# Optimization experiments

Measured on AMD Instinct MI355X. Metric: run time of the kernel, lower is better.

The kernel has to match this reference:

```python
import jax, jax.numpy as jnp
import numpy as np

D_MODEL = 1024

def setup_inputs() -> dict:
    key = jax.random.key(0)
    ks = jax.random.split(key, 7)
    B, T, D = 4, 4096, D_MODEL
    s = 1.0 / np.sqrt(D)
    return {
        "x": jax.random.normal(ks[0], (B, T, D), dtype=jnp.float32),
        "Wq": jax.random.normal(ks[1], (D, D), dtype=jnp.float32) * s,
        "bq": jax.random.normal(ks[2], (D,), dtype=jnp.float32) * 0.01,
        "Wk": jax.random.normal(ks[3], (D, D), dtype=jnp.float32) * s,
        "bk": jax.random.normal(ks[4], (D,), dtype=jnp.float32) * 0.01,
        "Wv": jax.random.normal(ks[5], (D, D), dtype=jnp.float32) * s,
        "bv": jax.random.normal(ks[6], (D,), dtype=jnp.float32) * 0.01,
    }

def reference(x, Wq, bq, Wk, bk, Wv, bv):
    # x: [B, T, D]; Linear weights stored [out, in] like torch -> x @ W.T + b
    D = x.shape[-1]
    T = x.shape[1]
    scale = jnp.sqrt(jnp.asarray(D, dtype=x.dtype))
    Q = jnp.einsum('btd,ed->bte', x, Wq) + bq
    K = jnp.einsum('btd,ed->bte', x, Wk) + bk
    V = jnp.einsum('btd,ed->bte', x, Wv) + bv
    scores = jnp.einsum('bqd,bkd->bqk', Q, K) / scale  # [B, T, T]
    causal = jnp.tril(jnp.ones((T, T), dtype=bool))    # True = keep (q >= k)
    neg_inf = jnp.asarray(-jnp.inf, dtype=scores.dtype)
    scores = jnp.where(causal, scores, neg_inf)
    probs = jax.nn.softmax(scores, axis=-1)
    return jnp.einsum('bqk,bkd->bqd', probs, V)
```

## Files before the change

### kernel.cpp

```cpp
#include <hip/hip_runtime.h>
#include <hip/hip_bf16.h>
#include <math.h>


typedef __bf16 bf16;
typedef __bf16 bf16x8 __attribute__((ext_vector_type(8)));
typedef float  f32x4  __attribute__((ext_vector_type(4)));

#define LOG2E 1.4426950408889634f

static constexpr size_t OFF_XB   = 0;
static constexpr size_t OFF_WQB  = 33554432;
static constexpr size_t OFF_WKB  = 35651584;
static constexpr size_t OFF_WVB  = 37748736;
static constexpr size_t OFF_Q    = 39845888;
static constexpr size_t OFF_K    = 73400320;
static constexpr size_t OFF_VT   = 106954752;
static constexpr size_t OFF_S    = 140509184;
static constexpr size_t OFF_PSUM = 209715200;
static constexpr size_t OFF_LINV = 211812352;

typedef __attribute__((address_space(1))) void gvoid_t;
typedef __attribute__((address_space(3))) void lvoid_t;

__device__ __forceinline__ void gload16(const void* g, void* l) {
  __builtin_amdgcn_global_load_lds((gvoid_t*)g, (lvoid_t*)l, 16, 0, 0);
}

#define PRIO1() __builtin_amdgcn_s_setprio(1)
#define PRIO0() __builtin_amdgcn_s_setprio(0)
#define BARF()  asm volatile("s_barrier" ::: "memory")
#define SB0()   __builtin_amdgcn_sched_barrier(0)
#define VM0()   asm volatile("s_waitcnt vmcnt(0)" ::: "memory")
#define VM4()   asm volatile("s_waitcnt vmcnt(4)" ::: "memory")

struct Ctx { int tid, lane, quad, col16, wr, wc, wcol; };
__device__ __forceinline__ Ctx mk_ctx() {
  Ctx c; c.tid = (int)threadIdx.x; c.lane = c.tid & 63;
  int w = c.tid >> 6;
  c.quad = c.lane >> 4; c.col16 = c.lane & 15;
  c.wr = (w >> 1) * 64; c.wc = (w & 1) * 64; c.wcol = w & 1;
  return c;
}

__device__ __forceinline__ void stage_tile(const bf16* g, long ld, bf16* s, int tid) {
  int lane = tid & 63, w = tid >> 6;
  const bf16* gp = g + (long)(lane >> 2) * ld + (long)(lane & 3) * 8;
  long step = 16 * ld;
  gload16(gp + (long)(2 * w) * step,     s + (2 * w) * 512);
  gload16(gp + (long)(2 * w + 1) * step, s + (2 * w + 1) * 512);
}

__device__ __forceinline__ void mfma_step(const bf16* sA, const bf16* sB,
                                          const Ctx& c, f32x4 acc[4][4]) {
  bf16x8 a[4], b[4];
#pragma unroll
  for (int i = 0; i < 4; ++i) {
    a[i] = *(const bf16x8*)(sA + ((c.wr + i * 16 + c.col16) * 32 + c.quad * 8));
    b[i] = *(const bf16x8*)(sB + ((c.wc + i * 16 + c.col16) * 32 + c.quad * 8));
  }
#pragma unroll
  for (int i = 0; i < 4; ++i)
#pragma unroll
    for (int j = 0; j < 4; ++j)
      acc[i][j] = __builtin_amdgcn_mfma_f32_16x16x32_bf16(a[i], b[j], acc[i][j], 0, 0, 0);
}

__device__ __forceinline__ void zero_acc(f32x4 acc[4][4]) {
  f32x4 z = {0.f, 0.f, 0.f, 0.f};
#pragma unroll
  for (int i = 0; i < 4; ++i)
#pragma unroll
    for (int j = 0; j < 4; ++j) acc[i][j] = z;
}

__device__ __forceinline__ int tridec(int i) {
  int qt = (int)((sqrtf(8.0f * (float)i + 1.0f) - 1.0f) * 0.5f);
  while ((qt + 1) * (qt + 2) / 2 <= i) ++qt;
  while (qt * (qt + 1) / 2 > i) --qt;
  return qt;
}

struct CC { int soff, ra0, ra1, rb0, rb1, lofs; };
__device__ __forceinline__ CC mk_cc(int tid) {
  CC c;
  int lane = tid & 63, w = tid >> 6;
  int quad = lane >> 4, col16 = lane & 15;
  int wrow = (w >> 2) << 7, wcol = (w & 3) << 6;
  int c7 = col16 & 7;
  c.soff = ((tid >> 3) << 10) + (((tid & 7) ^ ((tid >> 3) & 7)) << 3);
  c.ra0 = ((wrow + col16) << 6) + ((quad ^ c7) << 3);
  c.ra1 = ((wrow + col16) << 6) + (((4 | quad) ^ c7) << 3);
  c.rb0 = ((wcol + col16) << 6) + ((quad ^ c7) << 3);
  c.rb1 = ((wcol + col16) << 6) + (((4 | quad) ^ c7) << 3);
  c.lofs = w << 9;
  return c;
}

__device__ __forceinline__ void stg(const bf16* g, int kofs, bf16* l, const CC& c) {
  const bf16* g0 = g + kofs + c.soff;
  gload16(g0,         l + c.lofs);
  gload16(g0 + 65536, l + c.lofs + 4096);
}

__device__ __forceinline__ void read_a(const bf16* buf, const CC& c, int h, bf16x8 a[8]) {
#pragma unroll
  for (int f = 0; f < 4; ++f) {
    a[f * 2 + 0] = *(const bf16x8*)(buf + c.ra0 + h * 4096 + f * 1024);
    a[f * 2 + 1] = *(const bf16x8*)(buf + c.ra1 + h * 4096 + f * 1024);
  }
}

__device__ __forceinline__ void read_b(const bf16* buf, const CC& c, int cc, bf16x8 bb[4]) {
#pragma unroll
  for (int g = 0; g < 2; ++g) {
    bb[g * 2 + 0] = *(const bf16x8*)(buf + c.rb0 + cc * 2048 + g * 1024);
    bb[g * 2 + 1] = *(const bf16x8*)(buf + c.rb1 + cc * 2048 + g * 1024);
  }
}

__device__ __forceinline__ void read_ab(const bf16* bufA, const bf16* bufB,
                                        const CC& c, bf16x8 a[8], bf16x8 bb[4]) {
#pragma unroll
  for (int f = 0; f < 4; ++f) {
    a[f * 2 + 0] = *(const bf16x8*)(bufA + c.ra0 + f * 1024);
    a[f * 2 + 1] = *(const bf16x8*)(bufA + c.ra1 + f * 1024);
    if (f < 2) {
      bb[f * 2 + 0] = *(const bf16x8*)(bufB + c.rb0 + f * 1024);
      bb[f * 2 + 1] = *(const bf16x8*)(bufB + c.rb1 + f * 1024);
    }
  }
}

__device__ __forceinline__ void mfma16(const bf16x8 a[8], const bf16x8 bb[4],
                                       int h, int cc, f32x4 acc[8][4]) {
#pragma unroll
  for (int f = 0; f < 4; ++f)
#pragma unroll
    for (int g = 0; g < 2; ++g)
#pragma unroll
      for (int kk = 0; kk < 2; ++kk)
        acc[h * 4 + f][cc * 2 + g] = __builtin_amdgcn_mfma_f32_16x16x32_bf16(
            a[f * 2 + kk], bb[g * 2 + kk], acc[h * 4 + f][cc * 2 + g], 0, 0, 0);
}

__device__ __forceinline__ void zero8x4(f32x4 acc[8][4]) {
  f32x4 z = {0.f, 0.f, 0.f, 0.f};
#pragma unroll
  for (int i = 0; i < 8; ++i)
#pragma unroll
    for (int j = 0; j < 4; ++j) acc[i][j] = z;
}

template <int NT>
__device__ __forceinline__ void gemm256_core(const bf16* __restrict__ Ag,
                                             const bf16* __restrict__ Bg,
                                             bf16* sA0, bf16* sA1,
                                             bf16* sB0, bf16* sB1,
                                             const CC& c, f32x4 acc[8][4]) {
  stg(Ag, 0,           sA0, c); stg(Ag, 131072,      sA0 + 8192, c);
  stg(Bg, 0,           sB0, c); stg(Bg, 131072,      sB0 + 8192, c);
  stg(Bg, 64,          sB1, c); stg(Bg, 64 + 131072, sB1 + 8192, c);
  VM4();

  bf16x8 a[8], b0[4], b1[4];
#pragma unroll 1
  for (int i = 0; i < NT / 2 - 1; ++i) {
    const int k1 = (2 * i + 1) << 6, k2 = k1 + 64, k3 = k1 + 128;
    BARF();
    read_ab(sA0, sB0, c, a, b0);
    stg(Ag, k1, sA1, c);
    PRIO1(); mfma16(a, b0, 0, 0, acc); PRIO0(); SB0();
    BARF();
    read_b(sB0, c, 1, b1);
    stg(Ag, k1 + 131072, sA1 + 8192, c);
    PRIO1(); mfma16(a, b1, 0, 1, acc); PRIO0(); SB0();
    BARF();
    read_a(sA0, c, 1, a);
    stg(Bg, k2, sB0, c);
    PRIO1(); mfma16(a, b1, 1, 1, acc); PRIO0(); SB0();
    BARF();
    stg(Bg, k2 + 131072, sB0 + 8192, c);
    PRIO1(); mfma16(a, b0, 1, 0, acc); PRIO0();
    VM4(); SB0();
    BARF();
    read_ab(sA1, sB1, c, a, b0);
    stg(Ag, k2, sA0, c);
    PRIO1(); mfma16(a, b0, 0, 0, acc); PRIO0(); SB0();
    BARF();
    read_b(sB1, c, 1, b1);
    stg(Ag, k2 + 131072, sA0 + 8192, c);
    PRIO1(); mfma16(a, b1, 0, 1, acc); PRIO0(); SB0();
    BARF();
    read_a(sA1, c, 1, a);
    stg(Bg, k3, sB1, c);
    PRIO1(); mfma16(a, b1, 1, 1, acc); PRIO0(); SB0();
    BARF();
    stg(Bg, k3 + 131072, sB1 + 8192, c);
    PRIO1(); mfma16(a, b0, 1, 0, acc); PRIO0();
    VM4(); SB0();
  }
  {
    const int k1 = (NT - 1) << 6;
    BARF();
    read_ab(sA0, sB0, c, a, b0);
    stg(Ag, k1, sA1, c);
    PRIO1(); mfma16(a, b0, 0, 0, acc); PRIO0(); SB0();
    BARF();
    read_b(sB0, c, 1, b1);
    stg(Ag, k1 + 131072, sA1 + 8192, c);
    PRIO1(); mfma16(a, b1, 0, 1, acc); PRIO0(); SB0();
    BARF();
    read_a(sA0, c, 1, a);
    PRIO1(); mfma16(a, b1, 1, 1, acc); PRIO0(); SB0();
    PRIO1(); mfma16(a, b0, 1, 0, acc); PRIO0();
    VM0(); SB0();
    BARF();
    read_ab(sA1, sB1, c, a, b0);
    PRIO1(); mfma16(a, b0, 0, 0, acc); PRIO0(); SB0();
    BARF();
    read_b(sB1, c, 1, b1);
    PRIO1(); mfma16(a, b1, 0, 1, acc); PRIO0(); SB0();
    BARF();
    read_a(sA1, c, 1, a);
    PRIO1(); mfma16(a, b1, 1, 1, acc); PRIO0();
    mfma16(a, b0, 1, 0, acc);
  }
}


__global__ __launch_bounds__(256) void cvt_all(const float* __restrict__ x,
                                               const float* __restrict__ Wq,
                                               const float* __restrict__ Wk,
                                               const float* __restrict__ Wv,
                                               bf16* __restrict__ xb,
                                               bf16* __restrict__ wqb,
                                               bf16* __restrict__ wkb,
                                               bf16* __restrict__ wvb) {
  int b = (int)blockIdx.x;
  const float* in; bf16* out; long base;
  if (b < 8192)      { in = x;  out = xb;  base = (long)b * 2048; }
  else if (b < 8704) { in = Wq; out = wqb; base = (long)(b - 8192) * 2048; }
  else if (b < 9216) { in = Wk; out = wkb; base = (long)(b - 8704) * 2048; }
  else               { in = Wv; out = wvb; base = (long)(b - 9216) * 2048; }
  long i = base + (long)threadIdx.x * 8;
  float4 f0 = *(const float4*)(in + i);
  float4 f1 = *(const float4*)(in + i + 4);
  bf16x8 h;
  h[0] = (bf16)f0.x; h[1] = (bf16)f0.y; h[2] = (bf16)f0.z; h[3] = (bf16)f0.w;
  h[4] = (bf16)f1.x; h[5] = (bf16)f1.y; h[6] = (bf16)f1.z; h[7] = (bf16)f1.w;
  *(bf16x8*)(out + i) = h;
}

__global__ __launch_bounds__(512, 2) void qkv_gemm(const bf16* __restrict__ X,
                                                   const bf16* __restrict__ Wq,
                                                   const bf16* __restrict__ Wk,
                                                   const bf16* __restrict__ Wv,
                                                   const float* __restrict__ bq,
                                                   const float* __restrict__ bk,
                                                   const float* __restrict__ bv,
                                                   bf16* __restrict__ Q,
                                                   bf16* __restrict__ K,
                                                   bf16* __restrict__ Vt) {
  __shared__ __align__(16) bf16 lds[4][16384];
  const int tid = (int)threadIdx.x;
  const CC c = mk_cc(tid);
  int b0i = (int)blockIdx.x;
  int b = (b0i & 7) * 96 + (b0i >> 3);
  const bf16 *Ag, *Bg;
  const bool is_vt = (b >= 512);
  if (!is_vt) {
    int isK = b >> 8, rem = b & 255;
    Ag = X + (long)(rem >> 2) * 262144;
    Bg = (isK ? Wk : Wq) + (long)(rem & 3) * 262144;
  } else {
    int rem = b - 512;
    Ag = Wv + (long)((rem >> 4) & 3) * 262144;
    Bg = X + (long)(rem >> 6) * 4194304 + (long)(rem & 15) * 262144;
  }
  f32x4 acc[8][4];
  zero8x4(acc);
  gemm256_core<16>(Ag, Bg, lds[0], lds[1], lds[2], lds[3], c, acc);

  const int lane = tid & 63, w = tid >> 6;
  const int quad = lane >> 4, col16 = lane & 15;
  const int wrow = (w >> 2) << 7, wcol = (w & 3) << 6;
  if (!is_vt) {
    int isK = b >> 8, rem = b & 255;
    long r0 = (long)(rem >> 2) * 256, c0 = (long)(rem & 3) * 256;
    const float* bias = isK ? bk : bq;
    bf16* out = isK ? K : Q;
#pragma unroll
    for (int n = 0; n < 4; ++n) {
      int col = (int)c0 + wcol + (n >> 1) * 32 + (n & 1) * 16 + col16;
      float bb = bias[col];
#pragma unroll
      for (int m = 0; m < 8; ++m) {
        long rowb = r0 + wrow + (m >> 2) * 64 + (m & 3) * 16 + quad * 4;
#pragma unroll
        for (int r = 0; r < 4; ++r)
          out[(rowb + r) * 1024 + col] = (bf16)(acc[m][n][r] + bb);
      }
    }
  } else {
    int rem = b - 512;
    int z = rem >> 6;
    long r0 = (long)((rem >> 4) & 3) * 256, c0 = (long)(rem & 15) * 256;
    bf16* out = Vt + (long)z * 4194304;
#pragma unroll
    for (int m = 0; m < 8; ++m) {
      long rowb = r0 + wrow + (m >> 2) * 64 + (m & 3) * 16 + quad * 4;
      float bb[4];
#pragma unroll
      for (int r = 0; r < 4; ++r) bb[r] = bv[rowb + r];
#pragma unroll
      for (int n = 0; n < 4; ++n) {
        int col = (int)c0 + wcol + (n >> 1) * 32 + (n & 1) * 16 + col16;
#pragma unroll
        for (int r = 0; r < 4; ++r)
          out[(rowb + r) * 4096 + col] = (bf16)(acc[m][n][r] + bb[r]);
      }
    }
  }
}

__device__ __attribute__((noinline)) void s_tile(const bf16* __restrict__ Q,
                                                 const bf16* __restrict__ K,
                                                 bf16* __restrict__ S,
                                                 float* __restrict__ psum,
                                                 int b) {
  static __shared__ __align__(16) bf16 lds[4][16384];
  static __shared__ float sred[8][128];
  const int tid = (int)threadIdx.x;
  const CC c = mk_cc(tid);
  int z = b & 3, ti = b >> 2;
  int QT = tridec(ti);
  int KT = ti - QT * (QT + 1) / 2;
  const bf16* Ag = Q + (long)z * 4194304 + (long)QT * 262144;
  const bf16* Bg = K + (long)z * 4194304 + (long)KT * 262144;
  f32x4 acc[8][4];
  zero8x4(acc);
  gemm256_core<16>(Ag, Bg, lds[0], lds[1], lds[2], lds[3], c, acc);

  const int lane = tid & 63, w = tid >> 6;
  const int quad = lane >> 4, col16 = lane & 15;
  const int rh = w >> 2, ch = (w & 3) >> 1;
  const int wcol64 = (w & 1) << 6;
  const bool diag = (QT == KT);
  const bool skip = diag && (rh == 0) && (ch == 1);
  const bool mask = diag && (rh == ch);
  const int qt128 = 2 * QT + rh, kt128 = 2 * KT + ch;
  bf16* st = S + ((long)z * 528 + (long)(qt128 * (qt128 + 1) / 2 + kt128)) * 16384;
  float rs[8][4];
#pragma unroll
  for (int m = 0; m < 8; ++m)
#pragma unroll
    for (int rr = 0; rr < 4; ++rr) rs[m][rr] = 0.f;
#pragma unroll
  for (int m = 0; m < 8; ++m) {
    int row_l = (m >> 2) * 64 + (m & 3) * 16 + quad * 4;
#pragma unroll
    for (int n = 0; n < 4; ++n) {
      int col_l = wcol64 + (n >> 1) * 32 + (n & 1) * 16 + col16;
#pragma unroll
      for (int rr = 0; rr < 4; ++rr) {
        float p = exp2f(acc[m][n][rr] * (0.03125f * LOG2E));
        if (mask && col_l > row_l + rr) p = 0.0f;
        bf16 h = (bf16)p;
        if (!skip) st[(row_l + rr) * 128 + col_l] = h;
        rs[m][rr] += (float)h;
      }
    }
  }
#pragma unroll
  for (int m = 0; m < 8; ++m)
#pragma unroll
    for (int rr = 0; rr < 4; ++rr)
#pragma unroll
      for (int msk = 1; msk <= 8; msk <<= 1)
        rs[m][rr] += __shfl_xor(rs[m][rr], msk);
  if (col16 == 0) {
#pragma unroll
    for (int m = 0; m < 8; ++m)
#pragma unroll
      for (int rr = 0; rr < 4; ++rr)
        sred[w][(m >> 2) * 64 + (m & 3) * 16 + quad * 4 + rr] = rs[m][rr];
  }
  __syncthreads();
  {
    int rh2 = (tid >> 7) & 1, row_l = tid & 127, ch2 = tid >> 8;
    int base = rh2 * 4 + ch2 * 2;
    psum[((long)z * 4096 + (long)QT * 256 + rh2 * 128 + row_l) * 32 + 2 * KT + ch2] =
        sred[base][row_l] + sred[base + 1][row_l];
  }
}

__global__ __launch_bounds__(512, 2) void s_gemm(const bf16* __restrict__ Q,
                                                 const bf16* __restrict__ K,
                                                 bf16* __restrict__ S,
                                                 float* __restrict__ psum) {
  const int r = (int)blockIdx.x;
  s_tile(Q, K, S, psum, (r & 7) * 64 + (r >> 3));
  if (r < 32) {
    __syncthreads();
    s_tile(Q, K, S, psum, 512 + r);
  }
}

__global__ __launch_bounds__(256) void inv_sums(const float* __restrict__ psum,
                                                float* __restrict__ linv) {
  long i = (long)blockIdx.x * 256 + threadIdx.x;
  int q = (int)(i & 4095);
  int nt = (q >> 7) + 1;
  const float* ps = psum + i * 32;
  float l = 0.f;
  for (int t = 0; t < nt; ++t) l += ps[t];
  linv[i] = 1.0f / l;
}

__global__ __launch_bounds__(256) void o_gemm(const bf16* __restrict__ S,
                                              const bf16* __restrict__ Vt,
                                              const float* __restrict__ linv,
                                              float* __restrict__ out) {
  __shared__ __align__(16) bf16 sA[2][128 * 32], sB[2][128 * 32];
  Ctx c = mk_ctx();
  int b = (int)blockIdx.x;
  int z = b & 3, et = (b >> 2) & 7, q0i = (b >> 5) & 7, gen = b >> 8;
  int qt = (gen == 0) ? q0i : (gen == 1) ? 15 - q0i
         : (gen == 2) ? 16 + q0i : 31 - q0i;
  long q0 = (long)qt * 128, e0 = (long)et * 128;
  const bf16* Bb = Vt + (long)z * 4194304 + e0 * 4096;
  long tribase = ((long)z * 528 + (long)qt * (qt + 1) / 2) * 16384;
  f32x4 acc[4][4]; zero_acc(acc);
  int kend = (qt + 1) * 128;
  for (int k = 0; k < kend; k += 64) {
    const bf16* Ab = S + tribase + (long)(k >> 7) * 16384 + (k & 127);
    stage_tile(Ab,      128, sA[0], c.tid);
    stage_tile(Ab + 32, 128, sA[1], c.tid);
    stage_tile(Bb + k,      4096, sB[0], c.tid);
    stage_tile(Bb + k + 32, 4096, sB[1], c.tid);
    __syncthreads();
    mfma_step(sA[0], sB[0], c, acc);
    mfma_step(sA[1], sB[1], c, acc);
    __syncthreads();
  }
  long zq = (long)z * 4096 + q0;
#pragma unroll
  for (int i = 0; i < 4; ++i) {
    int rowb = c.wr + i * 16 + c.quad * 4;
    float li[4];
#pragma unroll
    for (int r = 0; r < 4; ++r) li[r] = linv[zq + rowb + r];
#pragma unroll
    for (int j = 0; j < 4; ++j) {
      int col = c.wc + j * 16 + c.col16;
#pragma unroll
      for (int r = 0; r < 4; ++r)
        out[(zq + rowb + r) * 1024 + e0 + col] = acc[i][j][r] * li[r];
    }
  }
}

extern "C" void kernel_launch(void* const* d_in, const int* in_sizes, int n_in,
                              void* d_out, int out_size, void* d_ws, size_t ws_size,
                              hipStream_t stream) {
  (void)in_sizes; (void)n_in; (void)out_size; (void)ws_size;
  const float* x  = (const float*)d_in[0];
  const float* Wq = (const float*)d_in[1];
  const float* bq = (const float*)d_in[2];
  const float* Wk = (const float*)d_in[3];
  const float* bk = (const float*)d_in[4];
  const float* Wv = (const float*)d_in[5];
  const float* bv = (const float*)d_in[6];

  char* ws = (char*)d_ws;
  bf16*  xb   = (bf16*)(ws + OFF_XB);
  bf16*  wqb  = (bf16*)(ws + OFF_WQB);
  bf16*  wkb  = (bf16*)(ws + OFF_WKB);
  bf16*  wvb  = (bf16*)(ws + OFF_WVB);
  bf16*  Qb   = (bf16*)(ws + OFF_Q);
  bf16*  Kb   = (bf16*)(ws + OFF_K);
  bf16*  Vtb  = (bf16*)(ws + OFF_VT);
  bf16*  Sb   = (bf16*)(ws + OFF_S);
  float* psum = (float*)(ws + OFF_PSUM);
  float* linv = (float*)(ws + OFF_LINV);

  cvt_all<<<9728, 256, 0, stream>>>(x, Wq, Wk, Wv, xb, wqb, wkb, wvb);
  qkv_gemm<<<768, 512, 0, stream>>>(xb, wqb, wkb, wvb, bq, bk, bv, Qb, Kb, Vtb);
  s_gemm<<<512, 512, 0, stream>>>(Qb, Kb, Sb, psum);
  inv_sums<<<64, 256, 0, stream>>>(psum, linv);
  o_gemm<<<1024, 256, 0, stream>>>(Sb, Vtb, linv, (float*)d_out);
}
```

Before: 505.6 us.

## Split diagonal score tiles into separate 128-tile kernel, skip masked upper tiles

The QK^T score kernel previously computed all 544 256x256 tiles including diagonal ones, where a quarter of the work was masked out, and 32 blocks ran a second tile serially. It now runs the 480 strictly-below-diagonal 256 tiles with no masking and handles the diagonal region in a separate kernel using 128x128 tiles, computing only the three needed sub-tiles per diagonal block. This removes the wasted upper-triangle compute and the tail imbalance from the two-tile blocks. It adds one extra kernel launch, and the diagonal kernel uses a smaller and possibly less efficient GEMM path.

```diff
diff --git a/kernel.cpp b/kernel.cpp
--- a/kernel.cpp
+++ b/kernel.cpp
@@ -324,18 +324,19 @@
   }
 }
 
-__device__ __attribute__((noinline)) void s_tile(const bf16* __restrict__ Q,
+__global__ __launch_bounds__(512, 2) void s_gemm(const bf16* __restrict__ Q,
                                                  const bf16* __restrict__ K,
                                                  bf16* __restrict__ S,
-                                                 float* __restrict__ psum,
-                                                 int b) {
-  static __shared__ __align__(16) bf16 lds[4][16384];
-  static __shared__ float sred[8][128];
+                                                 float* __restrict__ psum) {
+  __shared__ __align__(16) bf16 lds[4][16384];
+  __shared__ float sred[8][128];
   const int tid = (int)threadIdx.x;
   const CC c = mk_cc(tid);
-  int z = b & 3, ti = b >> 2;
-  int QT = tridec(ti);
-  int KT = ti - QT * (QT + 1) / 2;
+  int b0i = (int)blockIdx.x;
+  int bsw = (b0i & 7) * 60 + (b0i >> 3);
+  int z = bsw & 3, j = bsw >> 2;
+  int QT = tridec(j) + 1;
+  int KT = j - QT * (QT - 1) / 2;
   const bf16* Ag = Q + (long)z * 4194304 + (long)QT * 262144;
   const bf16* Bg = K + (long)z * 4194304 + (long)KT * 262144;
   f32x4 acc[8][4];
@@ -346,9 +347,6 @@
   const int quad = lane >> 4, col16 = lane & 15;
   const int rh = w >> 2, ch = (w & 3) >> 1;
   const int wcol64 = (w & 1) << 6;
-  const bool diag = (QT == KT);
-  const bool skip = diag && (rh == 0) && (ch == 1);
-  const bool mask = diag && (rh == ch);
   const int qt128 = 2 * QT + rh, kt128 = 2 * KT + ch;
   bf16* st = S + ((long)z * 528 + (long)(qt128 * (qt128 + 1) / 2 + kt128)) * 16384;
   float rs[8][4];
@@ -365,9 +363,8 @@
 #pragma unroll
       for (int rr = 0; rr < 4; ++rr) {
         float p = exp2f(acc[m][n][rr] * (0.03125f * LOG2E));
-        if (mask && col_l > row_l + rr) p = 0.0f;
         bf16 h = (bf16)p;
-        if (!skip) st[(row_l + rr) * 128 + col_l] = h;
+        st[(row_l + rr) * 128 + col_l] = h;
         rs[m][rr] += (float)h;
       }
     }
@@ -395,16 +392,71 @@
   }
 }
 
-__global__ __launch_bounds__(512, 2) void s_gemm(const bf16* __restrict__ Q,
-                                                 const bf16* __restrict__ K,
-                                                 bf16* __restrict__ S,
-                                                 float* __restrict__ psum) {
-  const int r = (int)blockIdx.x;
-  s_tile(Q, K, S, psum, (r & 7) * 64 + (r >> 3));
-  if (r < 32) {
+__global__ __launch_bounds__(256) void s_diag(const bf16* __restrict__ Q,
+                                              const bf16* __restrict__ K,
+                                              bf16* __restrict__ S,
+                                              float* __restrict__ psum) {
+  __shared__ __align__(16) bf16 sA[2][128 * 32], sB[2][128 * 32];
+  __shared__ float sred[2][128];
+  Ctx c = mk_ctx();
+  int d = (int)blockIdx.x;
+  int z = d & 3, u = d >> 2;
+  int Qq = u / 3, s = u % 3;
+  int qt = 2 * Qq + (s > 0 ? 1 : 0);
+  int kt = 2 * Qq + (s == 2 ? 1 : 0);
+  int ti = qt * (qt + 1) / 2 + kt;
+  long q0 = (long)qt * 128, k0 = (long)kt * 128;
+  const bf16* Ab = Q + (long)z * 4194304 + q0 * 1024;
+  const bf16* Bb = K + (long)z * 4194304 + k0 * 1024;
+  f32x4 acc[4][4]; zero_acc(acc);
+  for (int k = 0; k < 1024; k += 64) {
+    stage_tile(Ab + k,      1024, sA[0], c.tid);
+    stage_tile(Ab + k + 32, 1024, sA[1], c.tid);
+    stage_tile(Bb + k,      1024, sB[0], c.tid);
+    stage_tile(Bb + k + 32, 1024, sB[1], c.tid);
     __syncthreads();
-    s_tile(Q, K, S, psum, 512 + r);
-  }
+    mfma_step(sA[0], sB[0], c, acc);
+    mfma_step(sA[1], sB[1], c, acc);
+    __syncthreads();
+  }
+  bf16* st = S + ((long)z * 528 + ti) * 16384;
+  const bool diag = (qt == kt);
+  float rs[4][4];
+#pragma unroll
+  for (int i = 0; i < 4; ++i) {
+#pragma unroll
+    for (int r = 0; r < 4; ++r) {
+      int row_l = c.wr + i * 16 + c.quad * 4 + r;
+      float ssum = 0.f;
+#pragma unroll
+      for (int jj = 0; jj < 4; ++jj) {
+        int col_l = c.wc + jj * 16 + c.col16;
+        float p = exp2f(acc[i][jj][r] * (0.03125f * LOG2E));
+        if (diag && col_l > row_l) p = 0.0f;
+        bf16 h = (bf16)p;
+        st[row_l * 128 + col_l] = h;
+        ssum += (float)h;
+      }
+      rs[i][r] = ssum;
+    }
+  }
+#pragma unroll
+  for (int i = 0; i < 4; ++i)
+#pragma unroll
+    for (int r = 0; r < 4; ++r)
+#pragma unroll
+      for (int m = 1; m <= 8; m <<= 1)
+        rs[i][r] += __shfl_xor(rs[i][r], m);
+  if (c.col16 == 0) {
+#pragma unroll
+    for (int i = 0; i < 4; ++i)
+#pragma unroll
+      for (int r = 0; r < 4; ++r)
+        sred[c.wcol][c.wr + i * 16 + c.quad * 4 + r] = rs[i][r];
+  }
+  __syncthreads();
+  if (c.tid < 128)
+    psum[((long)z * 4096 + q0 + c.tid) * 32 + kt] = sred[0][c.tid] + sred[1][c.tid];
 }
 
 __global__ __launch_bounds__(256) void inv_sums(const float* __restrict__ psum,
@@ -487,7 +539,8 @@
 
   cvt_all<<<9728, 256, 0, stream>>>(x, Wq, Wk, Wv, xb, wqb, wkb, wvb);
   qkv_gemm<<<768, 512, 0, stream>>>(xb, wqb, wkb, wvb, bq, bk, bv, Qb, Kb, Vtb);
-  s_gemm<<<512, 512, 0, stream>>>(Qb, Kb, Sb, psum);
+  s_gemm<<<480, 512, 0, stream>>>(Qb, Kb, Sb, psum);
+  s_diag<<<192, 256, 0, stream>>>(Qb, Kb, Sb, psum);
   inv_sums<<<64, 256, 0, stream>>>(psum, linv);
   o_gemm<<<1024, 256, 0, stream>>>(Sb, Vtb, linv, (float*)d_out);
 }
```

Measured after the change: 489.5 us. -3.2%, faster.
